# Kernel tuning notes

Measured on AMD Instinct MI355X. Metric: run time of the kernel, lower is better.

The kernel has to match this reference:

```python
import jax, jax.numpy as jnp
import numpy as np

D = 256      # embedding_dim
K = 8192     # num_embeddings


def setup_inputs() -> dict:
    key = jax.random.key(0)
    k1, k2, k3, k4 = jax.random.split(key, 4)
    x = jax.random.normal(k1, (8, 4096, D), dtype=jnp.float32)
    W = jax.random.normal(k2, (D, D), dtype=jnp.float32) / np.sqrt(D)
    b = jax.random.normal(k3, (D,), dtype=jnp.float32) * 0.01
    codebook = jax.random.normal(k4, (K, D), dtype=jnp.float32)
    return {"x": x, "W": W, "b": b, "codebook": codebook}


def reference(x, W, b, codebook):
    # linear projection: z = x @ W^T + b  (torch nn.Linear convention)
    z = jnp.einsum('btd,ed->bte', x, W) + b            # [B,T,D]
    zf = z.reshape(-1, D)                               # [N,D]
    # squared L2 distances to codebook: ||z||^2 - 2 z.E^T + ||E||^2
    d2 = (jnp.sum(zf * zf, axis=1, keepdims=True)
          - 2.0 * zf @ codebook.T
          + jnp.sum(codebook * codebook, axis=1)[None, :])   # [N,K]
    idx = jnp.argmin(d2, axis=1)                        # [N]
    q = codebook[idx].reshape(z.shape)                  # [B,T,D]
    sg = jax.lax.stop_gradient
    dictionary_loss = jnp.mean((sg(z) - q) ** 2)
    commitment_loss = jnp.mean((z - sg(q)) ** 2)
    # straight-through estimator
    x_recon = z + sg(q - z)
    return x_recon, dictionary_loss, commitment_loss
```

## Files before the change

kernel.cpp:

```cpp
#include <hip/hip_runtime.h>

#define DIM   256
#define KCB   8192
#define NTOK  32768
#define NSPLIT 2
#define CPS   4096

using half8 = __attribute__((ext_vector_type(8))) _Float16;
using half4 = __attribute__((ext_vector_type(4))) _Float16;
using f32x4 = __attribute__((ext_vector_type(4))) float;

#define GLOBAL_AS(p) ((const __attribute__((address_space(1))) void*)(p))
#define LDS_AS(p)    ((__attribute__((address_space(3))) void*)(p))

__device__ __forceinline__ void ins2(float v, int i, float& b1v, int& b1i,
                                     float& b2v, int& b2i) {
    bool bet1 = (v < b1v) || (v == b1v && i < b1i);
    bool bet2 = (v < b2v) || (v == b2v && i < b2i);
    if (bet1) { b2v = b1v; b2i = b1i; b1v = v; b1i = i; }
    else if (bet2) { b2v = v; b2i = i; }
}

__global__ __launch_bounds__(256) void k_split(const float* __restrict__ src,
                                               _Float16* __restrict__ hi,
                                               _Float16* __restrict__ lo,
                                               float* __restrict__ norm, int nrows) {
    int row = (int)((blockIdx.x * blockDim.x + threadIdx.x) >> 6);
    int lane = threadIdx.x & 63;
    if (row >= nrows) return;
    float4 v = *(const float4*)&src[(size_t)row * DIM + lane * 4];
    float vv[4] = {v.x, v.y, v.z, v.w};
    half4 hh, hl;
    #pragma unroll
    for (int j = 0; j < 4; ++j) {
        _Float16 h = (_Float16)vv[j];
        hh[j] = h;
        hl[j] = (_Float16)(vv[j] - (float)h);
    }
    *(half4*)&hi[(size_t)row * DIM + lane * 4] = hh;
    if (lo) *(half4*)&lo[(size_t)row * DIM + lane * 4] = hl;
    if (norm) {
        float s = v.x*v.x + v.y*v.y + v.z*v.z + v.w*v.w;
        #pragma unroll
        for (int m = 32; m; m >>= 1) s += __shfl_xor(s, m);
        if (lane == 0) norm[row] = s;
    }
}

__global__ __launch_bounds__(256) void k_linear(const float* __restrict__ x,
                                                const _Float16* __restrict__ wh,
                                                const _Float16* __restrict__ wl,
                                                const float* __restrict__ bias,
                                                _Float16* __restrict__ zh,
                                                _Float16* __restrict__ zl) {
    const int tid = threadIdx.x;
    const int w = tid >> 6, lane = tid & 63;
    const int col = lane & 15, kg = lane >> 4;
    const int m0 = blockIdx.x * 64;
    const int e0 = w * 64;

    f32x4 acc[4][4];
    #pragma unroll
    for (int mi = 0; mi < 4; ++mi)
        #pragma unroll
        for (int nj = 0; nj < 4; ++nj) acc[mi][nj] = (f32x4){0.f, 0.f, 0.f, 0.f};

    for (int kc = 0; kc < 8; ++kc) {
        half8 ah[4], al[4], bh[4], bl[4];
        #pragma unroll
        for (int mi = 0; mi < 4; ++mi) {
            const float* p = &x[(size_t)(m0 + mi * 16 + col) * DIM + kc * 32 + kg * 8];
            float4 v0 = *(const float4*)p;
            float4 v1 = *(const float4*)(p + 4);
            float vv[8] = {v0.x, v0.y, v0.z, v0.w, v1.x, v1.y, v1.z, v1.w};
            #pragma unroll
            for (int j = 0; j < 8; ++j) {
                _Float16 h = (_Float16)vv[j];
                ah[mi][j] = h;
                al[mi][j] = (_Float16)(vv[j] - (float)h);
            }
        }
        #pragma unroll
        for (int nj = 0; nj < 4; ++nj) {
            size_t off = (size_t)(e0 + nj * 16 + col) * DIM + kc * 32 + kg * 8;
            bh[nj] = *(const half8*)&wh[off];
            bl[nj] = *(const half8*)&wl[off];
        }
        #pragma unroll
        for (int mi = 0; mi < 4; ++mi)
            #pragma unroll
            for (int nj = 0; nj < 4; ++nj) {
                acc[mi][nj] = __builtin_amdgcn_mfma_f32_16x16x32_f16(ah[mi], bh[nj], acc[mi][nj], 0, 0, 0);
                acc[mi][nj] = __builtin_amdgcn_mfma_f32_16x16x32_f16(ah[mi], bl[nj], acc[mi][nj], 0, 0, 0);
                acc[mi][nj] = __builtin_amdgcn_mfma_f32_16x16x32_f16(al[mi], bh[nj], acc[mi][nj], 0, 0, 0);
            }
    }
    #pragma unroll
    for (int nj = 0; nj < 4; ++nj) {
        int e = e0 + nj * 16 + col;
        float bv = bias[e];
        #pragma unroll
        for (int mi = 0; mi < 4; ++mi)
            #pragma unroll
            for (int r = 0; r < 4; ++r) {
                int m = m0 + mi * 16 + kg * 4 + r;
                float zv = acc[mi][nj][r] + bv;
                _Float16 h = (_Float16)zv;
                zh[(size_t)m * DIM + e] = h;
                zl[(size_t)m * DIM + e] = (_Float16)(zv - (float)h);
            }
    }
}

__global__ __launch_bounds__(256, 1) void k_argmin(const _Float16* __restrict__ zh,
                                                   const _Float16* __restrict__ ch,
                                                   const float* __restrict__ cnorm,
                                                   float4* __restrict__ cand) {
    extern __shared__ __align__(16) char smem[];
    const int tid = threadIdx.x;
    const int w = tid >> 6, lane = tid & 63;
    const int wm = w >> 1, wn = w & 1;
    const int col = lane & 15, kg = lane >> 4;
    const int split = blockIdx.x & 1;
    const int m0 = (blockIdx.x >> 1) * 128;

    #pragma unroll
    for (int j = 0; j < 16; ++j) {
        int s = j * 256 + w * 64 + lane;
        int row = s >> 5;
        int gp = s & 31;
        int g = gp ^ (row & 15);
        const _Float16* src = zh + (size_t)(m0 + row) * DIM + g * 8;
        __builtin_amdgcn_global_load_lds(GLOBAL_AS(src),
            LDS_AS(smem + j * 4096 + w * 1024), 16, 0, 0);
    }

    float val[16];
    unsigned pidx[8];
    #pragma unroll
    for (int s = 0; s < 16; ++s) val[s] = 3.4e38f;
    #pragma unroll
    for (int s = 0; s < 8; ++s) pidx[s] = 0xFFFFFFFFu;

    f32x4 acc[4][4];
    #pragma unroll
    for (int mi = 0; mi < 4; ++mi)
        #pragma unroll
        for (int nj = 0; nj < 4; ++nj) acc[mi][nj] = (f32x4){0.f, 0.f, 0.f, 0.f};

    const _Float16* zbuf = (const _Float16*)smem;
    const _Float16* bbuf = (const _Float16*)(smem + 65536);

    for (int nt = 0; nt < 32; ++nt) {
        #pragma unroll
        for (int ks = 0; ks < 4; ++ks) {
            __syncthreads();
            {
                const int n0 = split * CPS + nt * 128;
                #pragma unroll
                for (int j = 0; j < 4; ++j) {
                    int s = j * 256 + w * 64 + lane;
                    int row = s >> 3, q = s & 7;
                    int g8s = q ^ (row & 7);
                    const _Float16* src = ch + (size_t)(n0 + row) * DIM + ks * 64 + g8s * 8;
                    __builtin_amdgcn_global_load_lds(GLOBAL_AS(src),
                        LDS_AS(smem + 65536 + j * 4096 + w * 1024), 16, 0, 0);
                }
            }
            __syncthreads();

            __builtin_amdgcn_s_setprio(1);
            #pragma unroll
            for (int kk = 0; kk < 2; ++kk) {
                half8 a[4];
                #pragma unroll
                for (int mi = 0; mi < 4; ++mi) {
                    int row = wm * 64 + mi * 16 + col;
                    int g = ks * 8 + kk * 4 + kg;
                    a[mi] = *(const half8*)&zbuf[(size_t)row * 256 + ((g ^ col) << 3)];
                }
                #pragma unroll
                for (int nj = 0; nj < 4; ++nj) {
                    int r = wn * 64 + nj * 16 + col;
                    half8 b = *(const half8*)&bbuf[(size_t)r * 64 + (((kk * 4 + kg) ^ (col & 7)) << 3)];
                    #pragma unroll
                    for (int mi = 0; mi < 4; ++mi)
                        acc[mi][nj] = __builtin_amdgcn_mfma_f32_16x16x32_f16(a[mi], b, acc[mi][nj], 0, 0, 0);
                }
            }
            __builtin_amdgcn_s_setprio(0);

            if (ks == 3) {
                #pragma unroll
                for (int nj = 0; nj < 4; ++nj) {
                    int nl = nt * 128 + wn * 64 + nj * 16 + col;
                    float cn = cnorm[split * CPS + nl];
                    #pragma unroll
                    for (int mi = 0; mi < 4; ++mi)
                        #pragma unroll
                        for (int r2 = 0; r2 < 4; ++r2) {
                            float sc = fmaf(-2.0f, acc[mi][nj][r2], cn);
                            int s = mi * 4 + r2;
                            bool bb2 = sc < val[s];
                            unsigned p = pidx[s >> 1];
                            unsigned np = (s & 1) ? ((p & 0x0000FFFFu) | ((unsigned)nl << 16))
                                                  : ((p & 0xFFFF0000u) | (unsigned)nl);
                            val[s] = bb2 ? sc : val[s];
                            pidx[s >> 1] = bb2 ? np : p;
                        }
                }
                #pragma unroll
                for (int mi = 0; mi < 4; ++mi)
                    #pragma unroll
                    for (int nj = 0; nj < 4; ++nj) acc[mi][nj] = (f32x4){0.f, 0.f, 0.f, 0.f};
            }
        }
    }

    __syncthreads();

    float b1[16], b2[16]; int i1[16], i2[16];
    #pragma unroll
    for (int s = 0; s < 16; ++s) {
        unsigned p = pidx[s >> 1];
        int nl = (s & 1) ? (int)(p >> 16) : (int)(p & 0xFFFFu);
        b1[s] = val[s]; i1[s] = split * CPS + nl;
        b2[s] = 3.4e38f; i2[s] = 0x7ffffffe;
    }
    #pragma unroll
    for (int m = 1; m < 16; m <<= 1) {
        #pragma unroll
        for (int s = 0; s < 16; ++s) {
            float p1 = __shfl_xor(b1[s], m); int j1 = __shfl_xor(i1[s], m);
            float p2 = __shfl_xor(b2[s], m); int j2 = __shfl_xor(i2[s], m);
            ins2(p1, j1, b1[s], i1[s], b2[s], i2[s]);
            ins2(p2, j2, b1[s], i1[s], b2[s], i2[s]);
        }
    }
    float4* cbuf = (float4*)smem;
    if (col == 0) {
        #pragma unroll
        for (int s = 0; s < 16; ++s) {
            int mi = s >> 2, r = s & 3;
            int row = wm * 64 + mi * 16 + kg * 4 + r;
            float4 v; v.x = b1[s]; v.y = __int_as_float(i1[s]); v.z = b2[s]; v.w = __int_as_float(i2[s]);
            cbuf[row * 2 + wn] = v;
        }
    }
    __syncthreads();
    if (tid < 128) {
        float4 a = cbuf[tid * 2 + 0];
        float4 b = cbuf[tid * 2 + 1];
        float v1 = a.x; int j1 = __float_as_int(a.y);
        float v2 = a.z; int j2 = __float_as_int(a.w);
        ins2(b.x, __float_as_int(b.y), v1, j1, v2, j2);
        ins2(b.z, __float_as_int(b.w), v1, j1, v2, j2);
        float4 o; o.x = v1; o.y = __int_as_float(j1); o.z = v2; o.w = __int_as_float(j2);
        cand[(size_t)split * NTOK + m0 + tid] = o;
    }
}

__global__ __launch_bounds__(256) void k_finalize(const _Float16* __restrict__ zh,
                                                  const _Float16* __restrict__ zl,
                                                  const float* __restrict__ cb,
                                                  const float* __restrict__ cnorm,
                                                  const float4* __restrict__ cand,
                                                  float* __restrict__ out,
                                                  float* __restrict__ partials) {
    __shared__ float blk[4];
    const int tid = threadIdx.x;
    const int w = tid >> 6, lane = tid & 63;
    const int token = blockIdx.x * 4 + w;

    int ci[4];
    #pragma unroll
    for (int s = 0; s < NSPLIT; ++s) {
        float4 c = cand[(size_t)s * NTOK + token];
        ci[2 * s]     = __float_as_int(c.y);
        ci[2 * s + 1] = __float_as_int(c.w);
    }

    half4 hv = *(const half4*)&zh[(size_t)token * DIM + lane * 4];
    half4 lv = *(const half4*)&zl[(size_t)token * DIM + lane * 4];
    float z0 = (float)hv[0] + (float)lv[0];
    float z1 = (float)hv[1] + (float)lv[1];
    float z2 = (float)hv[2] + (float)lv[2];
    float z3 = (float)hv[3] + (float)lv[3];

    const float4* cb4 = (const float4*)cb;
    float best = 3.4e38f; int bi = 0x7fffffff;
    #pragma unroll
    for (int j = 0; j < 2 * NSPLIT; ++j) {
        int idx = ci[j];
        float4 e = cb4[(size_t)idx * 64 + lane];
        float d = z0 * e.x + z1 * e.y + z2 * e.z + z3 * e.w;
        #pragma unroll
        for (int m = 32; m; m >>= 1) d += __shfl_xor(d, m);
        float sc = cnorm[idx] - 2.0f * d;
        if (sc < best || (sc == best && idx < bi)) { best = sc; bi = idx; }
    }

    float4 q = cb4[(size_t)bi * 64 + lane];
    *(float4*)&out[(size_t)token * DIM + lane * 4] = q;

    float dx = z0 - q.x, dy = z1 - q.y, dz = z2 - q.z, dw = z3 - q.w;
    float ss = dx*dx + dy*dy + dz*dz + dw*dw;
    #pragma unroll
    for (int m = 32; m; m >>= 1) ss += __shfl_xor(ss, m);
    if (lane == 0) blk[w] = ss;
    __syncthreads();
    if (tid == 0) partials[blockIdx.x] = blk[0] + blk[1] + blk[2] + blk[3];
}

__global__ __launch_bounds__(256) void k_losses(const float* __restrict__ partials,
                                                float* __restrict__ out) {
    __shared__ float red[256];
    float s = 0.0f;
    for (int i = threadIdx.x; i < NTOK / 4; i += 256) s += partials[i];
    red[threadIdx.x] = s;
    __syncthreads();
    for (int off = 128; off; off >>= 1) {
        if ((int)threadIdx.x < off) red[threadIdx.x] += red[threadIdx.x + off];
        __syncthreads();
    }
    if (threadIdx.x == 0) {
        float l = red[0] / (float)((size_t)NTOK * DIM);
        out[(size_t)NTOK * DIM]     = l;
        out[(size_t)NTOK * DIM + 1] = l;
    }
}

extern "C" void kernel_launch(void* const* d_in, const int* in_sizes, int n_in,
                              void* d_out, int out_size, void* d_ws, size_t ws_size,
                              hipStream_t stream) {
    const float* x  = (const float*)d_in[0];
    const float* W  = (const float*)d_in[1];
    const float* b  = (const float*)d_in[2];
    const float* cb = (const float*)d_in[3];
    float* out = (float*)d_out;

    char* ws = (char*)d_ws;
    size_t off = 0;
    _Float16* zh = (_Float16*)(ws + off); off += (size_t)NTOK * DIM * 2;
    _Float16* zl = (_Float16*)(ws + off); off += (size_t)NTOK * DIM * 2;
    _Float16* ch = (_Float16*)(ws + off); off += (size_t)KCB * DIM * 2;
    _Float16* wh = (_Float16*)(ws + off); off += (size_t)DIM * DIM * 2;
    _Float16* wl = (_Float16*)(ws + off); off += (size_t)DIM * DIM * 2;
    float* cnorm = (float*)(ws + off);    off += (size_t)KCB * 4;
    float4* cand = (float4*)(ws + off);   off += (size_t)NSPLIT * NTOK * 16;
    float* parts = (float*)(ws + off);

    static hipError_t _attr_once = hipFuncSetAttribute(
        reinterpret_cast<const void*>(k_argmin),
        hipFuncAttributeMaxDynamicSharedMemorySize, 81920);
    (void)_attr_once;

    k_split<<<dim3(DIM / 4), 256, 0, stream>>>(W, wh, wl, nullptr, DIM);
    k_split<<<dim3(KCB / 4), 256, 0, stream>>>(cb, ch, nullptr, cnorm, KCB);
    k_linear<<<dim3(NTOK / 64), 256, 0, stream>>>(x, wh, wl, b, zh, zl);
    k_argmin<<<dim3(NTOK / 128 * NSPLIT), 256, 81920, stream>>>(zh, ch, cnorm, cand);
    k_finalize<<<dim3(NTOK / 4), 256, 0, stream>>>(zh, zl, cb, cnorm, cand, out, parts);
    k_losses<<<1, 256, 0, stream>>>(parts, out);
}
```

Baseline: 378.3 us.

## Double-buffer codebook tiles in LDS with async prefetch of next k-chunk

```diff
diff --git a/kernel.cpp b/kernel.cpp
--- a/kernel.cpp
+++ b/kernel.cpp
@@ -135,6 +135,34 @@
             LDS_AS(smem + j * 4096 + w * 1024), 16, 0, 0);
     }
 
+    size_t eb[2];
+    #pragma unroll
+    for (int j = 0; j < 2; ++j) {
+        int s  = j * 256 + w * 64 + lane;
+        int rr = s >> 3, q = s & 7;
+        int g2 = q ^ (rr & 7);
+        int r  = rr * 2 + (g2 >> 2);
+        int kg4 = g2 & 3;
+        eb[j] = (size_t)(split * CPS + r) * DIM + kg4 * 8;
+    }
+    int bslot[4];
+    #pragma unroll
+    for (int nj = 0; nj < 4; ++nj) {
+        int r = wn * 64 + nj * 16 + col;
+        bslot[nj] = (((r >> 1) << 3) + ((((r & 1) << 2) + kg) ^ ((r >> 1) & 7))) << 4;
+    }
+
+    auto STAGE = [&](int cc, int buf) {
+        size_t off = (size_t)(cc >> 3) * 128 * DIM + (cc & 7) * 32;
+        char* dst = smem + 65536 + buf * 8192 + w * 1024;
+        #pragma unroll
+        for (int j = 0; j < 2; ++j)
+            __builtin_amdgcn_global_load_lds(GLOBAL_AS(ch + eb[j] + off),
+                                             LDS_AS(dst + j * 4096), 16, 0, 0);
+    };
+
+    STAGE(0, 0);
+
     float val[16];
     unsigned pidx[8];
     #pragma unroll
@@ -149,48 +177,40 @@
         for (int nj = 0; nj < 4; ++nj) acc[mi][nj] = (f32x4){0.f, 0.f, 0.f, 0.f};
 
     const _Float16* zbuf = (const _Float16*)smem;
-    const _Float16* bbuf = (const _Float16*)(smem + 65536);
 
     for (int nt = 0; nt < 32; ++nt) {
         #pragma unroll
-        for (int ks = 0; ks < 4; ++ks) {
-            __syncthreads();
-            {
-                const int n0 = split * CPS + nt * 128;
+        for (int ks = 0; ks < 8; ++ks) {
+            const int c = nt * 8 + ks;
+            __builtin_amdgcn_s_barrier();
+            if (c < 255) {
+                STAGE(c + 1, (ks + 1) & 1);
+                asm volatile("s_waitcnt vmcnt(2)" ::: "memory");
+            } else {
+                asm volatile("s_waitcnt vmcnt(0)" ::: "memory");
+            }
+            __builtin_amdgcn_s_barrier();
+            __builtin_amdgcn_sched_barrier(0);
+
+            half8 a[4];
+            #pragma unroll
+            for (int mi = 0; mi < 4; ++mi) {
+                int row = wm * 64 + mi * 16 + col;
+                int g = ks * 4 + kg;
+                a[mi] = *(const half8*)&zbuf[(size_t)row * 256 + ((g ^ col) << 3)];
+            }
+            const char* bb = smem + 65536 + (ks & 1) * 8192;
+            __builtin_amdgcn_s_setprio(1);
+            #pragma unroll
+            for (int nj = 0; nj < 4; ++nj) {
+                half8 b = *(const half8*)(bb + bslot[nj]);
                 #pragma unroll
-                for (int j = 0; j < 4; ++j) {
-                    int s = j * 256 + w * 64 + lane;
-                    int row = s >> 3, q = s & 7;
-                    int g8s = q ^ (row & 7);
-                    const _Float16* src = ch + (size_t)(n0 + row) * DIM + ks * 64 + g8s * 8;
-                    __builtin_amdgcn_global_load_lds(GLOBAL_AS(src),
-                        LDS_AS(smem + 65536 + j * 4096 + w * 1024), 16, 0, 0);
-                }
-            }
-            __syncthreads();
-
-            __builtin_amdgcn_s_setprio(1);
-            #pragma unroll
-            for (int kk = 0; kk < 2; ++kk) {
-                half8 a[4];
-                #pragma unroll
-                for (int mi = 0; mi < 4; ++mi) {
-                    int row = wm * 64 + mi * 16 + col;
-                    int g = ks * 8 + kk * 4 + kg;
-                    a[mi] = *(const half8*)&zbuf[(size_t)row * 256 + ((g ^ col) << 3)];
-                }
-                #pragma unroll
-                for (int nj = 0; nj < 4; ++nj) {
-                    int r = wn * 64 + nj * 16 + col;
-                    half8 b = *(const half8*)&bbuf[(size_t)r * 64 + (((kk * 4 + kg) ^ (col & 7)) << 3)];
-                    #pragma unroll
-                    for (int mi = 0; mi < 4; ++mi)
-                        acc[mi][nj] = __builtin_amdgcn_mfma_f32_16x16x32_f16(a[mi], b, acc[mi][nj], 0, 0, 0);
-                }
+                for (int mi = 0; mi < 4; ++mi)
+                    acc[mi][nj] = __builtin_amdgcn_mfma_f32_16x16x32_f16(a[mi], b, acc[mi][nj], 0, 0, 0);
             }
             __builtin_amdgcn_s_setprio(0);
 
-            if (ks == 3) {
+            if (ks == 7) {
                 #pragma unroll
                 for (int nj = 0; nj < 4; ++nj) {
                     int nl = nt * 128 + wn * 64 + nj * 16 + col;
```

Result: no change. 378.5 us (+0.1%).
